# Kernel tuning notes

Hardware: AMD Instinct MI355X
Metric: run time of the kernel (lower is better)

Reference implementation:

```python
import jax, jax.numpy as jnp
import numpy as np

B, N, D = 1024, 8192, 128
BETA = 0.25


def setup_inputs() -> dict:
    key = jax.random.key(0)
    kx, kw = jax.random.split(key)
    x = jax.random.normal(kx, (B, D), dtype=jnp.float32)
    # nn.Embedding weight init: uniform(-1/num_embeddings, 1/num_embeddings)
    W = jax.random.uniform(kw, (N, D), dtype=jnp.float32, minval=-1.0 / N, maxval=1.0 / N)
    return {"x": x, "W": W}


def reference(x, W):
    # Squared L2 distances: (B, N) via expansion; single GEMM for the cross term.
    dist = (x * x).sum(axis=1, keepdims=True) - 2.0 * (x @ W.T) + (W * W).sum(axis=1)[None, :]
    # (-dist).topk(k=1) == argmin(dist); torch keeps the k dim -> ind is (B, 1)
    ind = jnp.argmin(dist, axis=1)[:, None]
    q = W[ind]  # (B, 1, D) codebook gather (matches torch embedding(ind) shape)
    # Faithful to source: (B, D) broadcasts against (B, 1, D) -> (B, B, D)
    loss = BETA * jnp.mean((x - jax.lax.stop_gradient(q)) ** 2) + jnp.mean((jax.lax.stop_gradient(x) - q) ** 2)
    quantized = x + jax.lax.stop_gradient(q - x)  # straight-through; (B, B, D) per source broadcast
    return quantized, ind, loss
```

## Files before the change

kernel.cpp:

```cpp
#include <hip/hip_runtime.h>
#include <stdint.h>

typedef float vfloat4 __attribute__((ext_vector_type(4)));

static const long long QN       = 134217728LL;
static const long long IND_OFF  = QN;
static const long long LOSS_OFF = QN + 1024;
static const long long PVAL_OFF = 1022LL * 131072 + 128;
static const long long PIDX_OFF = 1023LL * 131072 + 128;

#define WS_W2  0
#define WS_X2  8192
#define WS_SX  9216
#define WS_SQ  9344
#define WS_SQ2 9472

__global__ __launch_bounds__(256) void k_prep(const float* __restrict__ x,
                                              const float* __restrict__ W,
                                              float* __restrict__ ws) {
    const int b = blockIdx.x, tid = threadIdx.x;
    if (b < 36) {
        const float4* pr = (b < 32) ? ((const float4*)W + (size_t)(b * 256 + tid) * 32)
                                    : ((const float4*)x + (size_t)((b - 32) * 256 + tid) * 32);
        float s = 0.0f;
#pragma unroll 8
        for (int t = 0; t < 32; ++t) {
            float4 v = pr[t];
            s += v.x * v.x + v.y * v.y + v.z * v.z + v.w * v.w;
        }
        if (b < 32) ws[WS_W2 + b * 256 + tid] = s;
        else        ws[WS_X2 + (b - 32) * 256 + tid] = s;
    } else {
        __shared__ float sh[8][32];
        const int c = tid & 31, g = tid >> 5;
        const int col = (b - 36) * 32 + c;
        float sum = 0.0f;
        for (int r = g; r < 1024; r += 8) sum += x[(size_t)r * 128 + col];
        sh[g][c] = sum;
        __syncthreads();
        if (g == 0) {
            float t = 0.0f;
#pragma unroll
            for (int gg = 0; gg < 8; ++gg) t += sh[gg][c];
            ws[WS_SX + col] = t;
        }
        if (b == 36 && tid < 129) ws[WS_SQ + tid] = 0.0f;
    }
}

__global__ __launch_bounds__(256) void k_score(
    const float* __restrict__ x, const float* __restrict__ W,
    const float* __restrict__ w2, const float* __restrict__ x2,
    float* __restrict__ pval, int* __restrict__ pidx) {
    __shared__ float Xs[32][132];
    __shared__ float Wst[32][132];
    const int tid = threadIdx.x;
    const int tx = tid & 15, ty = tid >> 4;
    const int n0 = blockIdx.x * 128, m0 = blockIdx.y * 128;
    const float4* xv = (const float4*)x;
    const float4* wv = (const float4*)W;

    float acc[8][8];
#pragma unroll
    for (int i = 0; i < 8; ++i)
#pragma unroll
        for (int j = 0; j < 8; ++j) acc[i][j] = 0.0f;

    for (int kc = 0; kc < 4; ++kc) {
#pragma unroll
        for (int it = 0; it < 4; ++it) {
            int f = it * 256 + tid;
            int m = f >> 3, kq = f & 7;
            float4 a = xv[(size_t)(m0 + m) * 32 + kc * 8 + kq];
            float4 b = wv[(size_t)(n0 + m) * 32 + kc * 8 + kq];
            Xs[kq * 4 + 0][m] = a.x;
            Xs[kq * 4 + 1][m] = a.y;
            Xs[kq * 4 + 2][m] = a.z;
            Xs[kq * 4 + 3][m] = a.w;
            Wst[kq * 4 + 0][m] = b.x;
            Wst[kq * 4 + 1][m] = b.y;
            Wst[kq * 4 + 2][m] = b.z;
            Wst[kq * 4 + 3][m] = b.w;
        }
        __syncthreads();
#pragma unroll 8
        for (int k = 0; k < 32; ++k) {
            float4 a0 = *(const float4*)&Xs[k][ty * 8];
            float4 a1 = *(const float4*)&Xs[k][ty * 8 + 4];
            float4 b0 = *(const float4*)&Wst[k][tx * 8];
            float4 b1 = *(const float4*)&Wst[k][tx * 8 + 4];
            float af[8] = {a0.x, a0.y, a0.z, a0.w, a1.x, a1.y, a1.z, a1.w};
            float bf[8] = {b0.x, b0.y, b0.z, b0.w, b1.x, b1.y, b1.z, b1.w};
#pragma unroll
            for (int i = 0; i < 8; ++i)
#pragma unroll
                for (int j = 0; j < 8; ++j) acc[i][j] += af[i] * bf[j];
        }
        __syncthreads();
    }

    float w2v[8];
#pragma unroll
    for (int j = 0; j < 8; ++j) w2v[j] = w2[n0 + tx * 8 + j];

#pragma unroll
    for (int i = 0; i < 8; ++i) {
        const int row = m0 + ty * 8 + i;
        const float xxv = x2[row];
        float bestv;
        int besti = n0 + tx * 8;
        {
            float t = xxv - 2.0f * acc[i][0];
            bestv = t + w2v[0];
        }
#pragma unroll
        for (int j = 1; j < 8; ++j) {
            float t = xxv - 2.0f * acc[i][j];
            float s = t + w2v[j];
            if (s < bestv) { bestv = s; besti = n0 + tx * 8 + j; }
        }
        for (int off = 1; off < 16; off <<= 1) {
            float ov = __shfl_xor(bestv, off, 64);
            int oi = __shfl_xor(besti, off, 64);
            if (ov < bestv || (ov == bestv && oi < besti)) { bestv = ov; besti = oi; }
        }
        if (tx == 0) {
            pval[row * 64 + blockIdx.x] = bestv;
            pidx[row * 64 + blockIdx.x] = besti;
        }
    }
}

__global__ __launch_bounds__(256) void k_argmin(
    const float* __restrict__ W, const float* __restrict__ w2,
    const float* __restrict__ pval, const int* __restrict__ pidx,
    float* __restrict__ out, float* __restrict__ ws) {
    const int r = blockIdx.x * 256 + threadIdx.x;
    float bestv = pval[r * 64];
    int besti = pidx[r * 64];
    for (int c = 1; c < 64; ++c) {
        float v = pval[r * 64 + c];
        if (v < bestv) { bestv = v; besti = pidx[r * 64 + c]; }
    }
    out[IND_OFF + r] = (float)besti;

    float q2 = w2[besti];
    for (int off = 1; off < 64; off <<= 1) q2 += __shfl_xor(q2, off, 64);
    if ((threadIdx.x & 63) == 0) atomicAdd(ws + WS_SQ2, q2);

    float4* q = (float4*)out + (size_t)r * 32768;
    const float4* wr = (const float4*)W + (size_t)besti * 32;
    for (int t = 0; t < 32; ++t) {
        float4 v = wr[t];
        q[t] = v;
        float4 s = v;
        for (int off = 1; off < 64; off <<= 1) {
            s.x += __shfl_xor(s.x, off, 64);
            s.y += __shfl_xor(s.y, off, 64);
            s.z += __shfl_xor(s.z, off, 64);
            s.w += __shfl_xor(s.w, off, 64);
        }
        if ((threadIdx.x & 63) == 0) {
            atomicAdd(ws + WS_SQ + t * 4 + 0, s.x);
            atomicAdd(ws + WS_SQ + t * 4 + 1, s.y);
            atomicAdd(ws + WS_SQ + t * 4 + 2, s.z);
            atomicAdd(ws + WS_SQ + t * 4 + 3, s.w);
        }
    }
}

__global__ __launch_bounds__(256) void k_bcast(float* __restrict__ out,
                                               const float* __restrict__ ws) {
    const int bid = blockIdx.x, tid = threadIdx.x;
    if (bid == 0) {
        __shared__ float sh[256];
        float dotv = (tid < 128) ? ws[WS_SX + tid] * ws[WS_SQ + tid] : 0.0f;
        float sx2 = 0.0f;
        for (int r = tid; r < 1024; r += 256) sx2 += ws[WS_X2 + r];
        sh[tid] = dotv;
        __syncthreads();
        for (int s = 128; s > 0; s >>= 1) {
            if (tid < s) sh[tid] += sh[tid + s];
            __syncthreads();
        }
        const float dot = sh[0];
        __syncthreads();
        sh[tid] = sx2;
        __syncthreads();
        for (int s = 128; s > 0; s >>= 1) {
            if (tid < s) sh[tid] += sh[tid + s];
            __syncthreads();
        }
        if (tid == 0) {
            double Sx2 = (double)sh[0], Sq2 = (double)ws[WS_SQ2];
            double loss = 1.25 * (1024.0 * Sx2 + 1024.0 * Sq2 - 2.0 * (double)dot) / 134217728.0;
            out[LOSS_OFF] = (float)loss;
        }
        __syncthreads();
    }
    const int i = bid >> 2;
    const int quarter = bid & 3;
    const int t = tid & 31;
    const int jend = quarter * 256 + 256;
    const vfloat4* src = (const vfloat4*)out + (size_t)i * 32768;
    vfloat4 qv = src[t];
    vfloat4* dst = (vfloat4*)out + (size_t)i * 32768 + t;
    for (int j = quarter * 256 + (tid >> 5); j < jend; j += 8) {
        dst[(size_t)j * 32] = qv;
    }
}

extern "C" void kernel_launch(void* const* d_in, const int* in_sizes, int n_in,
                              void* d_out, int out_size, void* d_ws, size_t ws_size,
                              hipStream_t stream) {
    const float* x = (const float*)d_in[0];
    const float* W = (const float*)d_in[1];
    float* out = (float*)d_out;
    float* ws = (float*)d_ws;

    hipLaunchKernelGGL(k_prep, dim3(40), dim3(256), 0, stream, x, W, ws);
    hipLaunchKernelGGL(k_score, dim3(64, 8), dim3(256), 0, stream, x, W,
                       ws + WS_W2, ws + WS_X2, out + PVAL_OFF, (int*)(out + PIDX_OFF));
    hipLaunchKernelGGL(k_argmin, dim3(4), dim3(256), 0, stream, W, ws + WS_W2,
                       out + PVAL_OFF, (const int*)(out + PIDX_OFF), out, ws);
    hipLaunchKernelGGL(k_bcast, dim3(4096), dim3(256), 0, stream, out, ws);
}
```

Baseline: 635.9 us.

## Stage gathered codebook rows and partials in workspace, coalesce gather, widen broadcast grid

Per-row argmin partials and the gathered codebook rows now live in the workspace instead of scratch areas of the huge output. The gather is reorganised so 32 threads copy one row together, which coalesces the accesses. The column sums are done through shared memory, replacing the wave shuffles and many atomics. The broadcast kernel reads the compact gathered rows and uses twice as many blocks, each writing half as much, to raise parallelism on the memory-bound 512MB write.

```diff
diff --git a/kernel.cpp b/kernel.cpp
--- a/kernel.cpp
+++ b/kernel.cpp
@@ -6,14 +6,15 @@
 static const long long QN       = 134217728LL;
 static const long long IND_OFF  = QN;
 static const long long LOSS_OFF = QN + 1024;
-static const long long PVAL_OFF = 1022LL * 131072 + 128;
-static const long long PIDX_OFF = 1023LL * 131072 + 128;
-
-#define WS_W2  0
-#define WS_X2  8192
-#define WS_SX  9216
-#define WS_SQ  9344
-#define WS_SQ2 9472
+
+#define WS_W2    0
+#define WS_X2    8192
+#define WS_SX    9216
+#define WS_SQ    9344
+#define WS_SQ2   9472
+#define WS_PVAL  16384
+#define WS_PIDX  81920
+#define WS_Q     147456
 
 __global__ __launch_bounds__(256) void k_prep(const float* __restrict__ x,
                                               const float* __restrict__ W,
@@ -135,7 +136,10 @@
     const float* __restrict__ W, const float* __restrict__ w2,
     const float* __restrict__ pval, const int* __restrict__ pidx,
     float* __restrict__ out, float* __restrict__ ws) {
-    const int r = blockIdx.x * 256 + threadIdx.x;
+    __shared__ int sidx[256];
+    __shared__ float sh[2][128];
+    const int tid = threadIdx.x;
+    const int r = blockIdx.x * 256 + tid;
     float bestv = pval[r * 64];
     int besti = pidx[r * 64];
     for (int c = 1; c < 64; ++c) {
@@ -143,30 +147,29 @@
         if (v < bestv) { bestv = v; besti = pidx[r * 64 + c]; }
     }
     out[IND_OFF + r] = (float)besti;
+    sidx[tid] = besti;
 
     float q2 = w2[besti];
     for (int off = 1; off < 64; off <<= 1) q2 += __shfl_xor(q2, off, 64);
-    if ((threadIdx.x & 63) == 0) atomicAdd(ws + WS_SQ2, q2);
-
-    float4* q = (float4*)out + (size_t)r * 32768;
-    const float4* wr = (const float4*)W + (size_t)besti * 32;
-    for (int t = 0; t < 32; ++t) {
-        float4 v = wr[t];
-        q[t] = v;
-        float4 s = v;
-        for (int off = 1; off < 64; off <<= 1) {
-            s.x += __shfl_xor(s.x, off, 64);
-            s.y += __shfl_xor(s.y, off, 64);
-            s.z += __shfl_xor(s.z, off, 64);
-            s.w += __shfl_xor(s.w, off, 64);
-        }
-        if ((threadIdx.x & 63) == 0) {
-            atomicAdd(ws + WS_SQ + t * 4 + 0, s.x);
-            atomicAdd(ws + WS_SQ + t * 4 + 1, s.y);
-            atomicAdd(ws + WS_SQ + t * 4 + 2, s.z);
-            atomicAdd(ws + WS_SQ + t * 4 + 3, s.w);
-        }
-    }
+    if ((tid & 63) == 0) atomicAdd(ws + WS_SQ2, q2);
+    __syncthreads();
+
+    const int c4 = tid & 31, rg = tid >> 5;
+    float4* wsq = (float4*)(ws + WS_Q);
+    const float4* wv = (const float4*)W;
+#pragma unroll 4
+    for (int it = 0; it < 32; ++it) {
+        int rr = it * 8 + rg;
+        int idx = sidx[rr];
+        wsq[(size_t)(blockIdx.x * 256 + rr) * 32 + c4] = wv[(size_t)idx * 32 + c4];
+    }
+
+    const int d = tid & 127, g = tid >> 7;
+    float s = 0.0f;
+    for (int rr = g; rr < 256; rr += 2) s += W[(size_t)sidx[rr] * 128 + d];
+    sh[g][d] = s;
+    __syncthreads();
+    if (g == 0) atomicAdd(ws + WS_SQ + d, sh[0][d] + sh[1][d]);
 }
 
 __global__ __launch_bounds__(256) void k_bcast(float* __restrict__ out,
@@ -198,14 +201,14 @@
         }
         __syncthreads();
     }
-    const int i = bid >> 2;
-    const int quarter = bid & 3;
+    const int i = bid >> 3;
+    const int e = bid & 7;
     const int t = tid & 31;
-    const int jend = quarter * 256 + 256;
-    const vfloat4* src = (const vfloat4*)out + (size_t)i * 32768;
+    const vfloat4* src = (const vfloat4*)(ws + WS_Q) + (size_t)i * 32;
     vfloat4 qv = src[t];
     vfloat4* dst = (vfloat4*)out + (size_t)i * 32768 + t;
-    for (int j = quarter * 256 + (tid >> 5); j < jend; j += 8) {
+    const int jend = e * 128 + 128;
+    for (int j = e * 128 + (tid >> 5); j < jend; j += 8) {
         dst[(size_t)j * 32] = qv;
     }
 }
@@ -220,8 +223,8 @@
 
     hipLaunchKernelGGL(k_prep, dim3(40), dim3(256), 0, stream, x, W, ws);
     hipLaunchKernelGGL(k_score, dim3(64, 8), dim3(256), 0, stream, x, W,
-                       ws + WS_W2, ws + WS_X2, out + PVAL_OFF, (int*)(out + PIDX_OFF));
+                       ws + WS_W2, ws + WS_X2, ws + WS_PVAL, (int*)(ws + WS_PIDX));
     hipLaunchKernelGGL(k_argmin, dim3(4), dim3(256), 0, stream, W, ws + WS_W2,
-                       out + PVAL_OFF, (const int*)(out + PIDX_OFF), out, ws);
-    hipLaunchKernelGGL(k_bcast, dim3(4096), dim3(256), 0, stream, out, ws);
-}
+                       ws + WS_PVAL, (const int*)(ws + WS_PIDX), out, ws);
+    hipLaunchKernelGGL(k_bcast, dim3(8192), dim3(256), 0, stream, out, ws);
+}
```

After: 635.5 us. Within noise of the previous version (-0.1%).
